# Performance work log

Hardware: AMD Instinct MI355X
Metric: run time of the kernel (lower is better)

## Reference

```python
import jax, jax.numpy as jnp
import numpy as np

N_NODES = 100000
N_CELLS = 200000
N_EDGES = 300000
D = 128            # input_size == attention_size
HID = 128          # hidden width of custom_func MLP
SCALE = np.sqrt(np.float32(D))


def segment_softmax(src, seg_ids, num_segments):
    # src: [M, 1], seg_ids: [M] -> softmax normalized within each segment
    m = jax.ops.segment_max(src, seg_ids, num_segments=num_segments)
    e = jnp.exp(src - m[seg_ids])
    s = jax.ops.segment_sum(e, seg_ids, num_segments=num_segments)
    return e / s[seg_ids]


def setup_inputs() -> dict:
    key = jax.random.key(0)
    ks = jax.random.split(key, 9)
    cell_attr = jax.random.normal(ks[0], (N_CELLS, D), dtype=jnp.float32)
    edge_attr = jax.random.normal(ks[1], (N_EDGES, D), dtype=jnp.float32)
    node_embedding = jax.random.normal(ks[2], (N_NODES, D), dtype=jnp.float32)
    edge_index = jax.random.randint(ks[3], (2, N_EDGES), 0, N_NODES, dtype=jnp.int32)
    face = jax.random.randint(ks[4], (3, N_CELLS), 0, N_NODES, dtype=jnp.int32)
    # custom_func: 2-layer MLP (2D -> HID -> D)
    W1 = jax.random.normal(ks[5], (2 * D, HID), dtype=jnp.float32) / np.sqrt(2 * D)
    b1 = jnp.zeros((HID,), dtype=jnp.float32)
    W2 = jax.random.normal(ks[6], (HID, D), dtype=jnp.float32) / np.sqrt(HID)
    b2 = jnp.zeros((D,), dtype=jnp.float32)
    return {"cell_attr": cell_attr, "edge_attr": edge_attr,
            "node_embedding": node_embedding, "edge_index": edge_index,
            "face": face, "W1": W1, "b1": b1, "W2": W2, "b2": b2}


def reference(cell_attr, edge_attr, node_embedding, edge_index, face, W1, b1, W2, b2):
    senders, receivers = edge_index[0], edge_index[1]
    two_out = jnp.concatenate([receivers, senders], axis=0)   # outdegree order [2E]
    two_edge = jnp.concatenate([edge_attr, edge_attr], axis=0)  # [2E, D]

    # attention over edges grouped by target (outdegree) node
    att_src = jnp.sum(two_edge * node_embedding[two_out], axis=1, keepdims=True) / SCALE
    att = segment_softmax(att_src, two_out, N_NODES)            # [2E, 1]
    node_agg = jax.ops.segment_sum(two_edge * att, two_out, num_segments=N_NODES)  # [N, D]

    # cells gather mean of their 3 nodes
    cell_agg = (node_agg[face[0]] + node_agg[face[1]] + node_agg[face[2]]) / 3.0  # [C, D]

    # custom_func MLP on cat(cell_attr, cell_agg)
    h = jax.nn.relu(jnp.concatenate([cell_attr, cell_agg], axis=1) @ W1 + b1)
    cell_attr_new = h @ W2 + b2                                  # [C, D]

    # scatter_mean of cell features back to nodes
    cells_node_index = jnp.concatenate([face[0], face[1], face[2]], axis=0)  # [3C]
    tripled = jnp.concatenate([cell_attr_new] * 3, axis=0)                   # [3C, D]
    sums = jax.ops.segment_sum(tripled, cells_node_index, num_segments=N_NODES)
    counts = jax.ops.segment_sum(jnp.ones((3 * N_CELLS,), jnp.float32),
                                 cells_node_index, num_segments=N_NODES)
    node_attr = sums / jnp.maximum(counts, 1.0)[:, None]

    return cell_attr_new, node_attr
```

## Files before the change

kernel.cpp:

```cpp
#include <hip/hip_runtime.h>

#define NN 100000
#define NC 200000
#define NE 300000
#define D  128
#define NB 391
#define AB 37500
#define HB 2344

typedef unsigned short u16;
typedef __attribute__((ext_vector_type(8))) short bf16x8;
typedef __attribute__((ext_vector_type(4))) float f32x4;

__device__ __forceinline__ u16 f2bf(float x) {
    unsigned int u = __float_as_uint(x);
    u += 0x7fffu + ((u >> 16) & 1u);
    return (u16)(u >> 16);
}
__device__ __forceinline__ float bf2f(u16 h) {
    return __uint_as_float((unsigned int)h << 16);
}
__device__ __forceinline__ unsigned int cvt_pk_bf16(float a, float b) {
    unsigned int r;
    asm("v_cvt_pk_bf16_f32 %0, %1, %2" : "=v"(r) : "v"(a), "v"(b));
    return r;
}

#define MFMA16(a, b, c) __builtin_amdgcn_mfma_f32_16x16x32_bf16((a), (b), (c), 0, 0, 0)

__global__ __launch_bounds__(256) void k_att_prep(const float* __restrict__ edge_attr,
                                                  const float* __restrict__ emb,
                                                  const int* __restrict__ ei,
                                                  const int* __restrict__ face,
                                                  float* __restrict__ expv,
                                                  float* __restrict__ denom,
                                                  int* __restrict__ cntA,
                                                  int* __restrict__ cntF,
                                                  const float* __restrict__ W1,
                                                  const float* __restrict__ W2,
                                                  u16* __restrict__ w1h, u16* __restrict__ w1l,
                                                  u16* __restrict__ w2h, u16* __restrict__ w2l) {
    int b = blockIdx.x;
    int t = threadIdx.x;
    if (b < AB) {
        int lane = t & 63;
        int half = lane >> 5;
        int sub  = lane & 31;
        int e = b * 8 + (t >> 6) * 2 + half;
        int send = ei[e];
        int recv = ei[NE + e];
        float4 a  = ((const float4*)(edge_attr + (size_t)e * D))[sub];
        float4 r4 = ((const float4*)(emb + (size_t)recv * D))[sub];
        float4 s4 = ((const float4*)(emb + (size_t)send * D))[sub];
        float dr = a.x * r4.x + a.y * r4.y + a.z * r4.z + a.w * r4.w;
        float ds = a.x * s4.x + a.y * s4.y + a.z * s4.z + a.w * s4.w;
        #pragma unroll
        for (int off = 16; off > 0; off >>= 1) {
            dr += __shfl_xor(dr, off);
            ds += __shfl_xor(ds, off);
        }
        if (sub == 0) {
            const float inv_scale = 0.08838834764831845f;
            float er = __expf(dr * inv_scale);
            float es = __expf(ds * inv_scale);
            expv[e] = er;
            expv[NE + e] = es;
            atomicAdd(&denom[recv], er);
            atomicAdd(&denom[send], es);
        }
    } else if (b < AB + HB) {
        int i = (b - AB) * 256 + t;
        if (i >= 2 * NE) return;
        int tgt = (i < NE) ? ei[NE + i] : ei[i - NE];
        atomicAdd(&cntA[tgt], 1);
    } else if (b < AB + 2 * HB) {
        int i = (b - AB - HB) * 256 + t;
        if (i >= 3 * NC) return;
        atomicAdd(&cntF[face[i]], 1);
    } else {
        int tid = (b - AB - 2 * HB) * 256 + t;
        if (tid >= 6144) return;
        int l = tid & 63;
        int f = tid >> 6;
        const float* W; u16 *oh, *ol; int fi;
        if (f < 64) { W = W1; oh = w1h; ol = w1l; fi = f; }
        else        { W = W2; oh = w2h; ol = w2l; fi = f - 64; }
        int kt = fi >> 3, nt = fi & 7;
        int k0 = kt * 32 + 8 * (l >> 4);
        int n  = nt * 16 + (l & 15);
        #pragma unroll
        for (int i = 0; i < 8; i++) {
            float x = W[(size_t)(k0 + i) * 128 + n];
            u16 h = f2bf(x);
            oh[(size_t)fi * 512 + l * 8 + i] = h;
            ol[(size_t)fi * 512 + l * 8 + i] = f2bf(x - bf2f(h));
        }
    }
}

__global__ __launch_bounds__(256) void k_scan_blocks(const int* __restrict__ cntA,
                                                     const int* __restrict__ cntF,
                                                     int* __restrict__ bsumA,
                                                     int* __restrict__ bsumF) {
    __shared__ int s[256];
    int bb = blockIdx.x;
    bool fa = bb >= NB;
    const int* cnt = fa ? cntF : cntA;
    int* bsum = fa ? bsumF : bsumA;
    int blk = fa ? bb - NB : bb;
    int t = threadIdx.x;
    int i = blk * 256 + t;
    s[t] = (i < NN) ? cnt[i] : 0;
    __syncthreads();
    #pragma unroll
    for (int off = 128; off > 0; off >>= 1) {
        if (t < off) s[t] += s[t + off];
        __syncthreads();
    }
    if (t == 0) bsum[blk] = s[0];
}

__global__ __launch_bounds__(512) void k_scan_top(int* __restrict__ bsumA,
                                                  int* __restrict__ bsumF, int nb) {
    __shared__ int s[512];
    int* bsum = blockIdx.x ? bsumF : bsumA;
    int t = threadIdx.x;
    int v = (t < nb) ? bsum[t] : 0;
    s[t] = v;
    __syncthreads();
    #pragma unroll
    for (int off = 1; off < 512; off <<= 1) {
        int x = (t >= off) ? s[t - off] : 0;
        __syncthreads();
        s[t] += x;
        __syncthreads();
    }
    if (t < nb) bsum[t] = s[t] - v;
}

__global__ __launch_bounds__(256) void k_scan_final(const int* __restrict__ cntA,
                                                    const int* __restrict__ cntF,
                                                    const int* __restrict__ bsumA,
                                                    const int* __restrict__ bsumF,
                                                    int* __restrict__ offA,
                                                    int* __restrict__ offF) {
    __shared__ int s[256];
    int bb = blockIdx.x;
    bool fa = bb >= NB;
    const int* cnt = fa ? cntF : cntA;
    const int* bsum = fa ? bsumF : bsumA;
    int* off_out = fa ? offF : offA;
    int total = fa ? 3 * NC : 2 * NE;
    int blk = fa ? bb - NB : bb;
    int t = threadIdx.x;
    int i = blk * 256 + t;
    int v = (i < NN) ? cnt[i] : 0;
    s[t] = v;
    __syncthreads();
    #pragma unroll
    for (int off = 1; off < 256; off <<= 1) {
        int x = (t >= off) ? s[t - off] : 0;
        __syncthreads();
        s[t] += x;
        __syncthreads();
    }
    if (i < NN) off_out[i] = s[t] - v + bsum[blk];
    if (i == 0) off_out[NN] = total;
}

__global__ __launch_bounds__(256) void k_fill(const int* __restrict__ ei,
                                              const float* __restrict__ expv,
                                              const int* __restrict__ face,
                                              const int* __restrict__ offA,
                                              const int* __restrict__ offF,
                                              int* __restrict__ curA,
                                              int* __restrict__ curF,
                                              int* __restrict__ slotsA,
                                              float* __restrict__ wexpA,
                                              int* __restrict__ slotsF) {
    int b = blockIdx.x;
    int t = threadIdx.x;
    if (b < HB) {
        int i = b * 256 + t;
        if (i >= 2 * NE) return;
        int tgt = (i < NE) ? ei[NE + i] : ei[i - NE];
        int pos = offA[tgt] + atomicAdd(&curA[tgt], 1);
        slotsA[pos] = (i < NE) ? i : i - NE;
        wexpA[pos] = expv[i];
    } else {
        int i = (b - HB) * 256 + t;
        if (i >= 3 * NC) return;
        int tgt = face[i];
        int pos = offF[tgt] + atomicAdd(&curF[tgt], 1);
        int c = i; if (c >= NC) c -= NC; if (c >= NC) c -= NC;
        slotsF[pos] = c;
    }
}

__global__ __launch_bounds__(256) void k_agg_gather(const float* __restrict__ edge_attr,
                                                    const float* __restrict__ wexp,
                                                    const float* __restrict__ denom,
                                                    const int* __restrict__ offs,
                                                    const int* __restrict__ slots,
                                                    float* __restrict__ na) {
    int n = blockIdx.x * 4 + (threadIdx.x >> 6);
    int lane = threadIdx.x & 63;
    int half = lane >> 5, sub = lane & 31;
    if (n >= NN) return;
    int s0 = offs[n], s1 = offs[n + 1];
    float4 acc = {0.f, 0.f, 0.f, 0.f};
    for (int s = s0 + half; s < s1; s += 2) {
        int row = slots[s];
        float w = wexp[s];
        float4 a = ((const float4*)(edge_attr + (size_t)row * D))[sub];
        acc.x += w * a.x; acc.y += w * a.y; acc.z += w * a.z; acc.w += w * a.w;
    }
    acc.x += __shfl_xor(acc.x, 32);
    acc.y += __shfl_xor(acc.y, 32);
    acc.z += __shfl_xor(acc.z, 32);
    acc.w += __shfl_xor(acc.w, 32);
    if (half == 0) {
        float inv = (s1 > s0) ? 1.f / denom[n] : 0.f;
        float4 r; r.x = acc.x * inv; r.y = acc.y * inv; r.z = acc.z * inv; r.w = acc.w * inv;
        ((float4*)(na + (size_t)n * D))[sub] = r;
    }
}

__global__ __launch_bounds__(256) void k_smean_gather(const float* __restrict__ cell_out,
                                                      const int* __restrict__ offs,
                                                      const int* __restrict__ slots,
                                                      float* __restrict__ node_out) {
    int n = blockIdx.x * 4 + (threadIdx.x >> 6);
    int lane = threadIdx.x & 63;
    int half = lane >> 5, sub = lane & 31;
    if (n >= NN) return;
    int s0 = offs[n], s1 = offs[n + 1];
    float4 acc = {0.f, 0.f, 0.f, 0.f};
    for (int s = s0 + half; s < s1; s += 2) {
        int c = slots[s];
        float4 y = ((const float4*)(cell_out + (size_t)c * D))[sub];
        acc.x += y.x; acc.y += y.y; acc.z += y.z; acc.w += y.w;
    }
    acc.x += __shfl_xor(acc.x, 32);
    acc.y += __shfl_xor(acc.y, 32);
    acc.z += __shfl_xor(acc.z, 32);
    acc.w += __shfl_xor(acc.w, 32);
    if (half == 0) {
        int deg = s1 - s0;
        float inv = deg ? 1.f / (float)deg : 0.f;
        float4 r; r.x = acc.x * inv; r.y = acc.y * inv; r.z = acc.z * inv; r.w = acc.w * inv;
        ((float4*)(node_out + (size_t)n * D))[sub] = r;
    }
}

__device__ __forceinline__ void stage_split(char* lds, int row, int col8, const float* v) {
    unsigned int byte = ((unsigned int)row << 9) + ((unsigned int)col8 << 4);
    byte ^= (unsigned int)(row & 7) << 4;
    uint4 hi, lo;
    unsigned int* hp = (unsigned int*)&hi;
    unsigned int* lp = (unsigned int*)&lo;
    #pragma unroll
    for (int i = 0; i < 4; i++) {
        unsigned int h = cvt_pk_bf16(v[2 * i], v[2 * i + 1]);
        float h0 = __uint_as_float(h << 16);
        float h1 = __uint_as_float(h & 0xffff0000u);
        hp[i] = h;
        lp[i] = cvt_pk_bf16(v[2 * i] - h0, v[2 * i + 1] - h1);
    }
    *(uint4*)(lds + byte)         = hi;
    *(uint4*)(lds + 16384 + byte) = lo;
}

__global__ __launch_bounds__(256, 4) void k_mlp(const float* __restrict__ cell_attr,
                                                const float* __restrict__ na,
                                                const int* __restrict__ face,
                                                const u16* __restrict__ w1h,
                                                const u16* __restrict__ w1l,
                                                const u16* __restrict__ w2h,
                                                const u16* __restrict__ w2l,
                                                const float* __restrict__ b1,
                                                const float* __restrict__ b2,
                                                float* __restrict__ out) {
    __shared__ char lds[32768];
    const int t  = threadIdx.x;
    const int c0 = blockIdx.x * 32;

    {
        const int r = t >> 3;
        const int q = t & 7;
        float v[16];
        const float* pa = cell_attr + (size_t)(c0 + r) * D + q * 16;
        #pragma unroll
        for (int i = 0; i < 4; i++) *(float4*)(v + 4 * i) = *(const float4*)(pa + 4 * i);
        stage_split(lds, r, q * 2,     v);
        stage_split(lds, r, q * 2 + 1, v + 8);

        const int cid = c0 + r;
        const int f0 = face[cid], f1 = face[NC + cid], f2 = face[2 * NC + cid];
        const float* p0 = na + (size_t)f0 * D + q * 16;
        const float* p1 = na + (size_t)f1 * D + q * 16;
        const float* p2 = na + (size_t)f2 * D + q * 16;
        const float third = 1.f / 3.f;
        #pragma unroll
        for (int i = 0; i < 4; i++) {
            float4 a0 = *(const float4*)(p0 + 4 * i);
            float4 a1 = *(const float4*)(p1 + 4 * i);
            float4 a2 = *(const float4*)(p2 + 4 * i);
            v[4 * i + 0] = (a0.x + a1.x + a2.x) * third;
            v[4 * i + 1] = (a0.y + a1.y + a2.y) * third;
            v[4 * i + 2] = (a0.z + a1.z + a2.z) * third;
            v[4 * i + 3] = (a0.w + a1.w + a2.w) * third;
        }
        stage_split(lds, r, 16 + q * 2, v);
        stage_split(lds, r, 17 + q * 2, v + 8);
    }
    __syncthreads();

    const int w  = t >> 6;
    const int l  = t & 63;
    const int lr = l & 15;
    const int lg = l >> 4;
    const unsigned int swz = (unsigned int)(lr & 7) << 4;
    const size_t wl8 = (size_t)l * 8;
    const f32x4 z4 = {0.f, 0.f, 0.f, 0.f};
    f32x4 acc[2][2] = {{z4, z4}, {z4, z4}};

    {
        const unsigned int abase = ((unsigned int)lr << 9) + ((unsigned int)lg << 4);
        const u16* pW1h = w1h + (size_t)(w * 2) * 512 + wl8;
        const u16* pW1l = w1l + (size_t)(w * 2) * 512 + wl8;
        #pragma unroll 2
        for (int kt = 0; kt < 8; ++kt) {
            unsigned int ab = (abase + (unsigned int)kt * 64) ^ swz;
            bf16x8 aH0 = *(const bf16x8*)(lds + ab);
            bf16x8 aL0 = *(const bf16x8*)(lds + 16384 + ab);
            bf16x8 aH1 = *(const bf16x8*)(lds + ab + 8192);
            bf16x8 aL1 = *(const bf16x8*)(lds + 16384 + ab + 8192);
            #pragma unroll
            for (int jn = 0; jn < 2; ++jn) {
                size_t fo = (size_t)(kt * 8 + jn) * 512;
                bf16x8 bH = *(const bf16x8*)(pW1h + fo);
                bf16x8 bL = *(const bf16x8*)(pW1l + fo);
                acc[0][jn] = MFMA16(aH0, bL, acc[0][jn]);
                acc[0][jn] = MFMA16(aL0, bH, acc[0][jn]);
                acc[0][jn] = MFMA16(aH0, bH, acc[0][jn]);
                acc[1][jn] = MFMA16(aH1, bL, acc[1][jn]);
                acc[1][jn] = MFMA16(aL1, bH, acc[1][jn]);
                acc[1][jn] = MFMA16(aH1, bH, acc[1][jn]);
            }
        }
    }

    __syncthreads();

    {
        const int col0 = w * 32 + lr;
        const int col1 = col0 + 16;
        const float bb0 = b1[col0];
        const float bb1 = b1[col1];
        #pragma unroll
        for (int rt = 0; rt < 2; ++rt) {
            #pragma unroll
            for (int r = 0; r < 4; ++r) {
                int row = rt * 16 + lg * 4 + r;
                float h0 = fmaxf(acc[rt][0][r] + bb0, 0.f);
                float h1 = fmaxf(acc[rt][1][r] + bb1, 0.f);
                unsigned int ph = cvt_pk_bf16(h0, h1);
                float f0 = __uint_as_float(ph << 16);
                float f1 = __uint_as_float(ph & 0xffff0000u);
                unsigned int pl = cvt_pk_bf16(h0 - f0, h1 - f1);
                unsigned int swzr = (unsigned int)(row & 7) << 4;
                unsigned int b0 = (((unsigned int)row << 8) + ((unsigned int)col0 << 1)) ^ swzr;
                unsigned int bcol1 = (((unsigned int)row << 8) + ((unsigned int)col1 << 1)) ^ swzr;
                *(u16*)(lds + b0)            = (u16)ph;
                *(u16*)(lds + bcol1)         = (u16)(ph >> 16);
                *(u16*)(lds + 8192 + b0)     = (u16)pl;
                *(u16*)(lds + 8192 + bcol1)  = (u16)(pl >> 16);
            }
        }
    }
    __syncthreads();

    f32x4 acc2[2][2] = {{z4, z4}, {z4, z4}};
    {
        const unsigned int abase = ((unsigned int)lr << 8) + ((unsigned int)lg << 4);
        const u16* pW2h = w2h + (size_t)(w * 2) * 512 + wl8;
        const u16* pW2l = w2l + (size_t)(w * 2) * 512 + wl8;
        #pragma unroll 2
        for (int kt = 0; kt < 4; ++kt) {
            unsigned int ab = (abase + (unsigned int)kt * 64) ^ swz;
            bf16x8 aH0 = *(const bf16x8*)(lds + ab);
            bf16x8 aL0 = *(const bf16x8*)(lds + 8192 + ab);
            bf16x8 aH1 = *(const bf16x8*)(lds + ab + 4096);
            bf16x8 aL1 = *(const bf16x8*)(lds + 8192 + ab + 4096);
            #pragma unroll
            for (int jn = 0; jn < 2; ++jn) {
                size_t fo = (size_t)(kt * 8 + jn) * 512;
                bf16x8 bH = *(const bf16x8*)(pW2h + fo);
                bf16x8 bL = *(const bf16x8*)(pW2l + fo);
                acc2[0][jn] = MFMA16(aH0, bL, acc2[0][jn]);
                acc2[0][jn] = MFMA16(aL0, bH, acc2[0][jn]);
                acc2[0][jn] = MFMA16(aH0, bH, acc2[0][jn]);
                acc2[1][jn] = MFMA16(aH1, bL, acc2[1][jn]);
                acc2[1][jn] = MFMA16(aL1, bH, acc2[1][jn]);
                acc2[1][jn] = MFMA16(aH1, bH, acc2[1][jn]);
            }
        }
    }

    #pragma unroll
    for (int jn = 0; jn < 2; ++jn) {
        int col = w * 32 + jn * 16 + lr;
        float bb = b2[col];
        #pragma unroll
        for (int rt = 0; rt < 2; ++rt) {
            #pragma unroll
            for (int r = 0; r < 4; ++r) {
                int row = c0 + rt * 16 + lg * 4 + r;
                out[(size_t)row * D + col] = acc2[rt][jn][r] + bb;
            }
        }
    }
}

extern "C" void kernel_launch(void* const* d_in, const int* in_sizes, int n_in,
                              void* d_out, int out_size, void* d_ws, size_t ws_size,
                              hipStream_t stream) {
    (void)in_sizes; (void)n_in; (void)out_size; (void)ws_size;
    const float* cell_attr = (const float*)d_in[0];
    const float* edge_attr = (const float*)d_in[1];
    const float* emb       = (const float*)d_in[2];
    const int*   ei        = (const int*)d_in[3];
    const int*   face      = (const int*)d_in[4];
    const float* W1        = (const float*)d_in[5];
    const float* b1        = (const float*)d_in[6];
    const float* W2        = (const float*)d_in[7];
    const float* b2        = (const float*)d_in[8];

    float* out_cell = (float*)d_out;
    float* out_node = out_cell + (size_t)NC * D;

    float* denom  = (float*)d_ws;
    int*   cntA   = (int*)d_ws + NN;
    int*   cntF   = cntA + NN;
    int*   curA   = cntF + NN;
    int*   curF   = curA + NN;
    float* expv   = (float*)(curF + NN);
    int*   offA   = (int*)(expv + 2 * NE);
    int*   offF   = offA + NN + 1;
    int*   slotsA = offF + NN + 1;
    int*   slotsF = slotsA + 2 * NE;
    float* wexpA  = (float*)(slotsF + 3 * NC);
    int*   bsumA  = (int*)(wexpA + 2 * NE);
    int*   bsumF  = bsumA + 512;
    u16* w1h = (u16*)(((uintptr_t)(bsumF + 512) + 15) & ~(uintptr_t)15);
    u16* w1l = w1h + 64 * 512;
    u16* w2h = w1l + 64 * 512;
    u16* w2l = w2h + 32 * 512;

    hipMemsetAsync(d_ws, 0, (size_t)5 * NN * 4, stream);

    k_att_prep<<<AB + 2 * HB + 24, 256, 0, stream>>>(edge_attr, emb, ei, face, expv, denom,
                                                     cntA, cntF, W1, W2, w1h, w1l, w2h, w2l);

    k_scan_blocks<<<2 * NB, 256, 0, stream>>>(cntA, cntF, bsumA, bsumF);
    k_scan_top   <<<2, 512, 0, stream>>>(bsumA, bsumF, NB);
    k_scan_final <<<2 * NB, 256, 0, stream>>>(cntA, cntF, bsumA, bsumF, offA, offF);

    k_fill<<<2 * HB, 256, 0, stream>>>(ei, expv, face, offA, offF, curA, curF,
                                       slotsA, wexpA, slotsF);

    k_agg_gather<<<(NN + 3) / 4, 256, 0, stream>>>(edge_attr, wexpA, denom, offA, slotsA, out_node);

    k_mlp<<<NC / 32, 256, 0, stream>>>(cell_attr, out_node, face,
                                       w1h, w1l, w2h, w2l, b1, b2, out_cell);

    k_smean_gather<<<(NN + 3) / 4, 256, 0, stream>>>(out_cell, offF, slotsF, out_node);
}
```

Baseline: 690.6 us.

## Grid-stride attention prep, pack slot/weight pairs, full-wave shuffle-broadcast gathers

The attention-score kernel moves from one block per 8 edges to a fixed grid of 2048 blocks that grid-stride, with each half-wave handling two edges per iteration to raise memory-level parallelism. The CSR fill now writes slot index and exp weight as one packed int2, so one load replaces two separate arrays. Both gather kernels let a full wave cooperatively load up to 64 slot entries, broadcast them with shuffles, and issue four independent float2 row loads per step instead of half-wave float4 loads with a cross-half reduction. The goal is fewer index loads and more in-flight loads. The cost is narrower per-lane loads and serialized chunk loops for high-degree nodes.

New measurement: 665.8 us. 1.04x faster.

```diff
diff --git a/kernel.cpp b/kernel.cpp
--- a/kernel.cpp
+++ b/kernel.cpp
@@ -5,7 +5,7 @@
 #define NE 300000
 #define D  128
 #define NB 391
-#define AB 37500
+#define ATT_B 2048
 #define HB 2344
 
 typedef unsigned short u16;
@@ -42,43 +42,65 @@
                                                   u16* __restrict__ w2h, u16* __restrict__ w2l) {
     int b = blockIdx.x;
     int t = threadIdx.x;
-    if (b < AB) {
-        int lane = t & 63;
-        int half = lane >> 5;
-        int sub  = lane & 31;
-        int e = b * 8 + (t >> 6) * 2 + half;
-        int send = ei[e];
-        int recv = ei[NE + e];
-        float4 a  = ((const float4*)(edge_attr + (size_t)e * D))[sub];
-        float4 r4 = ((const float4*)(emb + (size_t)recv * D))[sub];
-        float4 s4 = ((const float4*)(emb + (size_t)send * D))[sub];
-        float dr = a.x * r4.x + a.y * r4.y + a.z * r4.z + a.w * r4.w;
-        float ds = a.x * s4.x + a.y * s4.y + a.z * s4.z + a.w * s4.w;
-        #pragma unroll
-        for (int off = 16; off > 0; off >>= 1) {
-            dr += __shfl_xor(dr, off);
-            ds += __shfl_xor(ds, off);
-        }
-        if (sub == 0) {
-            const float inv_scale = 0.08838834764831845f;
-            float er = __expf(dr * inv_scale);
-            float es = __expf(ds * inv_scale);
-            expv[e] = er;
-            expv[NE + e] = es;
-            atomicAdd(&denom[recv], er);
-            atomicAdd(&denom[send], es);
-        }
-    } else if (b < AB + HB) {
-        int i = (b - AB) * 256 + t;
+    if (b < ATT_B) {
+        const int HW = ATT_B * 8;
+        int hw  = b * 8 + (t >> 5);
+        int sub = t & 31;
+        const float inv_scale = 0.08838834764831845f;
+        for (int e0 = hw; e0 < NE; e0 += 2 * HW) {
+            int e1 = e0 + HW;
+            bool h1 = (e1 < NE);
+            int sd0 = ei[e0], rc0 = ei[NE + e0];
+            int sd1 = h1 ? ei[e1] : 0;
+            int rc1 = h1 ? ei[NE + e1] : 0;
+            float4 a0 = ((const float4*)(edge_attr + (size_t)e0 * D))[sub];
+            float4 r0 = ((const float4*)(emb + (size_t)rc0 * D))[sub];
+            float4 s0 = ((const float4*)(emb + (size_t)sd0 * D))[sub];
+            float dr0 = a0.x * r0.x + a0.y * r0.y + a0.z * r0.z + a0.w * r0.w;
+            float ds0 = a0.x * s0.x + a0.y * s0.y + a0.z * s0.z + a0.w * s0.w;
+            float dr1 = 0.f, ds1 = 0.f;
+            if (h1) {
+                float4 a1 = ((const float4*)(edge_attr + (size_t)e1 * D))[sub];
+                float4 r1 = ((const float4*)(emb + (size_t)rc1 * D))[sub];
+                float4 s1 = ((const float4*)(emb + (size_t)sd1 * D))[sub];
+                dr1 = a1.x * r1.x + a1.y * r1.y + a1.z * r1.z + a1.w * r1.w;
+                ds1 = a1.x * s1.x + a1.y * s1.y + a1.z * s1.z + a1.w * s1.w;
+            }
+            #pragma unroll
+            for (int off = 16; off > 0; off >>= 1) {
+                dr0 += __shfl_xor(dr0, off);
+                ds0 += __shfl_xor(ds0, off);
+                dr1 += __shfl_xor(dr1, off);
+                ds1 += __shfl_xor(ds1, off);
+            }
+            if (sub == 0) {
+                float er = __expf(dr0 * inv_scale);
+                float es = __expf(ds0 * inv_scale);
+                expv[e0] = er;
+                expv[NE + e0] = es;
+                atomicAdd(&denom[rc0], er);
+                atomicAdd(&denom[sd0], es);
+                if (h1) {
+                    float er1 = __expf(dr1 * inv_scale);
+                    float es1 = __expf(ds1 * inv_scale);
+                    expv[e1] = er1;
+                    expv[NE + e1] = es1;
+                    atomicAdd(&denom[rc1], er1);
+                    atomicAdd(&denom[sd1], es1);
+                }
+            }
+        }
+    } else if (b < ATT_B + HB) {
+        int i = (b - ATT_B) * 256 + t;
         if (i >= 2 * NE) return;
         int tgt = (i < NE) ? ei[NE + i] : ei[i - NE];
         atomicAdd(&cntA[tgt], 1);
-    } else if (b < AB + 2 * HB) {
-        int i = (b - AB - HB) * 256 + t;
+    } else if (b < ATT_B + 2 * HB) {
+        int i = (b - ATT_B - HB) * 256 + t;
         if (i >= 3 * NC) return;
         atomicAdd(&cntF[face[i]], 1);
     } else {
-        int tid = (b - AB - 2 * HB) * 256 + t;
+        int tid = (b - ATT_B - 2 * HB) * 256 + t;
         if (tid >= 6144) return;
         int l = tid & 63;
         int f = tid >> 6;
@@ -175,8 +197,7 @@
                                               const int* __restrict__ offF,
                                               int* __restrict__ curA,
                                               int* __restrict__ curF,
-                                              int* __restrict__ slotsA,
-                                              float* __restrict__ wexpA,
+                                              int2* __restrict__ swA,
                                               int* __restrict__ slotsF) {
     int b = blockIdx.x;
     int t = threadIdx.x;
@@ -185,8 +206,10 @@
         if (i >= 2 * NE) return;
         int tgt = (i < NE) ? ei[NE + i] : ei[i - NE];
         int pos = offA[tgt] + atomicAdd(&curA[tgt], 1);
-        slotsA[pos] = (i < NE) ? i : i - NE;
-        wexpA[pos] = expv[i];
+        int2 p;
+        p.x = (i < NE) ? i : i - NE;
+        p.y = __float_as_int(expv[i]);
+        swA[pos] = p;
     } else {
         int i = (b - HB) * 256 + t;
         if (i >= 3 * NC) return;
@@ -198,32 +221,51 @@
 }
 
 __global__ __launch_bounds__(256) void k_agg_gather(const float* __restrict__ edge_attr,
-                                                    const float* __restrict__ wexp,
+                                                    const int2* __restrict__ swA,
                                                     const float* __restrict__ denom,
                                                     const int* __restrict__ offs,
-                                                    const int* __restrict__ slots,
                                                     float* __restrict__ na) {
     int n = blockIdx.x * 4 + (threadIdx.x >> 6);
     int lane = threadIdx.x & 63;
-    int half = lane >> 5, sub = lane & 31;
     if (n >= NN) return;
     int s0 = offs[n], s1 = offs[n + 1];
-    float4 acc = {0.f, 0.f, 0.f, 0.f};
-    for (int s = s0 + half; s < s1; s += 2) {
-        int row = slots[s];
-        float w = wexp[s];
-        float4 a = ((const float4*)(edge_attr + (size_t)row * D))[sub];
-        acc.x += w * a.x; acc.y += w * a.y; acc.z += w * a.z; acc.w += w * a.w;
-    }
-    acc.x += __shfl_xor(acc.x, 32);
-    acc.y += __shfl_xor(acc.y, 32);
-    acc.z += __shfl_xor(acc.z, 32);
-    acc.w += __shfl_xor(acc.w, 32);
-    if (half == 0) {
-        float inv = (s1 > s0) ? 1.f / denom[n] : 0.f;
-        float4 r; r.x = acc.x * inv; r.y = acc.y * inv; r.z = acc.z * inv; r.w = acc.w * inv;
-        ((float4*)(na + (size_t)n * D))[sub] = r;
-    }
+    int deg = s1 - s0;
+    float2 acc = {0.f, 0.f};
+    int base = 0;
+    while (base < deg) {
+        int chunk = deg - base;
+        if (chunk > 64) chunk = 64;
+        int sl = 0; float wl = 0.f;
+        if (lane < chunk) {
+            int2 p = swA[s0 + base + lane];
+            sl = p.x;
+            wl = __int_as_float(p.y);
+        }
+        int j = 0;
+        for (; j + 4 <= chunk; j += 4) {
+            int r0 = __shfl(sl, j),     r1 = __shfl(sl, j + 1);
+            int r2 = __shfl(sl, j + 2), r3 = __shfl(sl, j + 3);
+            float w0 = __shfl(wl, j),     w1 = __shfl(wl, j + 1);
+            float w2 = __shfl(wl, j + 2), w3 = __shfl(wl, j + 3);
+            float2 a0 = ((const float2*)(edge_attr + (size_t)r0 * D))[lane];
+            float2 a1 = ((const float2*)(edge_attr + (size_t)r1 * D))[lane];
+            float2 a2 = ((const float2*)(edge_attr + (size_t)r2 * D))[lane];
+            float2 a3 = ((const float2*)(edge_attr + (size_t)r3 * D))[lane];
+            acc.x += w0 * a0.x + w1 * a1.x + w2 * a2.x + w3 * a3.x;
+            acc.y += w0 * a0.y + w1 * a1.y + w2 * a2.y + w3 * a3.y;
+        }
+        for (; j < chunk; ++j) {
+            int rr = __shfl(sl, j);
+            float ww = __shfl(wl, j);
+            float2 a = ((const float2*)(edge_attr + (size_t)rr * D))[lane];
+            acc.x += ww * a.x;
+            acc.y += ww * a.y;
+        }
+        base += chunk;
+    }
+    float inv = (deg > 0) ? 1.f / denom[n] : 0.f;
+    float2 r; r.x = acc.x * inv; r.y = acc.y * inv;
+    ((float2*)(na + (size_t)n * D))[lane] = r;
 }
 
 __global__ __launch_bounds__(256) void k_smean_gather(const float* __restrict__ cell_out,
@@ -232,25 +274,38 @@
                                                       float* __restrict__ node_out) {
     int n = blockIdx.x * 4 + (threadIdx.x >> 6);
     int lane = threadIdx.x & 63;
-    int half = lane >> 5, sub = lane & 31;
     if (n >= NN) return;
     int s0 = offs[n], s1 = offs[n + 1];
-    float4 acc = {0.f, 0.f, 0.f, 0.f};
-    for (int s = s0 + half; s < s1; s += 2) {
-        int c = slots[s];
-        float4 y = ((const float4*)(cell_out + (size_t)c * D))[sub];
-        acc.x += y.x; acc.y += y.y; acc.z += y.z; acc.w += y.w;
-    }
-    acc.x += __shfl_xor(acc.x, 32);
-    acc.y += __shfl_xor(acc.y, 32);
-    acc.z += __shfl_xor(acc.z, 32);
-    acc.w += __shfl_xor(acc.w, 32);
-    if (half == 0) {
-        int deg = s1 - s0;
-        float inv = deg ? 1.f / (float)deg : 0.f;
-        float4 r; r.x = acc.x * inv; r.y = acc.y * inv; r.z = acc.z * inv; r.w = acc.w * inv;
-        ((float4*)(node_out + (size_t)n * D))[sub] = r;
-    }
+    int deg = s1 - s0;
+    float2 acc = {0.f, 0.f};
+    int base = 0;
+    while (base < deg) {
+        int chunk = deg - base;
+        if (chunk > 64) chunk = 64;
+        int sl = 0;
+        if (lane < chunk) sl = slots[s0 + base + lane];
+        int j = 0;
+        for (; j + 4 <= chunk; j += 4) {
+            int c0 = __shfl(sl, j),     c1 = __shfl(sl, j + 1);
+            int c2 = __shfl(sl, j + 2), c3 = __shfl(sl, j + 3);
+            float2 y0 = ((const float2*)(cell_out + (size_t)c0 * D))[lane];
+            float2 y1 = ((const float2*)(cell_out + (size_t)c1 * D))[lane];
+            float2 y2 = ((const float2*)(cell_out + (size_t)c2 * D))[lane];
+            float2 y3 = ((const float2*)(cell_out + (size_t)c3 * D))[lane];
+            acc.x += y0.x + y1.x + y2.x + y3.x;
+            acc.y += y0.y + y1.y + y2.y + y3.y;
+        }
+        for (; j < chunk; ++j) {
+            int cc = __shfl(sl, j);
+            float2 y = ((const float2*)(cell_out + (size_t)cc * D))[lane];
+            acc.x += y.x;
+            acc.y += y.y;
+        }
+        base += chunk;
+    }
+    float inv = deg ? 1.f / (float)deg : 0.f;
+    float2 r; r.x = acc.x * inv; r.y = acc.y * inv;
+    ((float2*)(node_out + (size_t)n * D))[lane] = r;
 }
 
 __device__ __forceinline__ void stage_split(char* lds, int row, int col8, const float* v) {
@@ -448,29 +503,27 @@
     float* expv   = (float*)(curF + NN);
     int*   offA   = (int*)(expv + 2 * NE);
     int*   offF   = offA + NN + 1;
-    int*   slotsA = offF + NN + 1;
-    int*   slotsF = slotsA + 2 * NE;
-    float* wexpA  = (float*)(slotsF + 3 * NC);
-    int*   bsumA  = (int*)(wexpA + 2 * NE);
+    int*   bsumA  = offF + NN + 1;
     int*   bsumF  = bsumA + 512;
-    u16* w1h = (u16*)(((uintptr_t)(bsumF + 512) + 15) & ~(uintptr_t)15);
+    int*   slotsF = bsumF + 512;
+    int2*  swA    = (int2*)(((uintptr_t)(slotsF + 3 * NC) + 7) & ~(uintptr_t)7);
+    u16* w1h = (u16*)(((uintptr_t)(swA + 2 * NE) + 15) & ~(uintptr_t)15);
     u16* w1l = w1h + 64 * 512;
     u16* w2h = w1l + 64 * 512;
     u16* w2l = w2h + 32 * 512;
 
     hipMemsetAsync(d_ws, 0, (size_t)5 * NN * 4, stream);
 
-    k_att_prep<<<AB + 2 * HB + 24, 256, 0, stream>>>(edge_attr, emb, ei, face, expv, denom,
-                                                     cntA, cntF, W1, W2, w1h, w1l, w2h, w2l);
+    k_att_prep<<<ATT_B + 2 * HB + 24, 256, 0, stream>>>(edge_attr, emb, ei, face, expv, denom,
+                                                        cntA, cntF, W1, W2, w1h, w1l, w2h, w2l);
 
     k_scan_blocks<<<2 * NB, 256, 0, stream>>>(cntA, cntF, bsumA, bsumF);
     k_scan_top   <<<2, 512, 0, stream>>>(bsumA, bsumF, NB);
     k_scan_final <<<2 * NB, 256, 0, stream>>>(cntA, cntF, bsumA, bsumF, offA, offF);
 
-    k_fill<<<2 * HB, 256, 0, stream>>>(ei, expv, face, offA, offF, curA, curF,
-                                       slotsA, wexpA, slotsF);
-
-    k_agg_gather<<<(NN + 3) / 4, 256, 0, stream>>>(edge_attr, wexpA, denom, offA, slotsA, out_node);
+    k_fill<<<2 * HB, 256, 0, stream>>>(ei, expv, face, offA, offF, curA, curF, swA, slotsF);
+
+    k_agg_gather<<<(NN + 3) / 4, 256, 0, stream>>>(edge_attr, swA, denom, offA, out_node);
 
     k_mlp<<<NC / 32, 256, 0, stream>>>(cell_attr, out_node, face,
                                        w1h, w1l, w2h, w2l, b1, b2, out_cell);
```
